# Kernel optimization log

Measured on AMD Instinct MI355X. Metric: run time of the kernel, lower is better.

Reference implementation:

```python
import jax, jax.numpy as jnp
import numpy as np

B, N, D = 4, 2048, 1024
HEADS, DIM_HEAD = 16, 64
INNER = HEADS * DIM_HEAD  # 1024
SCALE = DIM_HEAD ** -0.5


def setup_inputs() -> dict:
    key = jax.random.key(0)
    ks = jax.random.split(key, 8)
    w = 0.02
    return {
        "x":  jax.random.normal(ks[0], (B, N, D), dtype=jnp.float32),
        "Wq": jax.random.normal(ks[1], (D, INNER), dtype=jnp.float32) * w,
        "bq": jax.random.normal(ks[2], (INNER,), dtype=jnp.float32) * w,
        "Wv": jax.random.normal(ks[3], (D, INNER), dtype=jnp.float32) * w,
        "bv": jax.random.normal(ks[4], (INNER,), dtype=jnp.float32) * w,
        "Wo": jax.random.normal(ks[5], (INNER, D), dtype=jnp.float32) * w,
        "bo": jax.random.normal(ks[6], (D,), dtype=jnp.float32) * w,
    }


def reference(x, Wq, bq, Wv, bv, Wo, bo):
    b, n, _ = x.shape
    q = x @ Wq + bq                      # [b, n, inner]
    v = x @ Wv + bv                      # [b, n, inner]
    # split heads -> [b, h, n, d]
    q = q.reshape(b, n, HEADS, DIM_HEAD).transpose(0, 2, 1, 3).astype(jnp.float32)
    v = v.reshape(b, n, HEADS, DIM_HEAD).transpose(0, 2, 1, 3)
    # k = q (self L2 attention)
    AB = jnp.einsum('bhid,bhjd->bhij', q, q)          # [b, h, n, n]
    AA = jnp.sum(q * q, axis=-1, keepdims=True)       # [b, h, n, 1]
    BB = jnp.swapaxes(AA, -1, -2)                     # [b, h, 1, n]
    sim = -(AA - 2.0 * AB + BB) * SCALE               # negative scaled L2 distance
    attn = jax.nn.softmax(sim, axis=-1)
    out = jnp.einsum('bhij,bhjd->bhid', attn, v)      # [b, h, n, d]
    out = out.transpose(0, 2, 1, 3).reshape(b, n, INNER)
    return out @ Wo + bo
```

## Files before the change

kernel.cpp:

```cpp
#include <hip/hip_runtime.h>
#include <hip/hip_bf16.h>

#define SEQ 2048
#define SCALE 0.125f
#define LOG2E 1.4426950408889634f

typedef __bf16 bf16;
typedef __bf16 bf16x4 __attribute__((ext_vector_type(4)));
typedef __bf16 bf16x8 __attribute__((ext_vector_type(8)));
typedef float f32x4 __attribute__((ext_vector_type(4)));
typedef unsigned int u32;

__device__ __forceinline__ void gl_lds16(const void* g, void* l) {
    __builtin_amdgcn_global_load_lds((const __attribute__((address_space(1))) u32*)g,
                                     (__attribute__((address_space(3))) u32*)l, 16, 0, 0);
}


__global__ __launch_bounds__(256) void k_cast_x(const float4* __restrict__ x,
                                                bf16x4* __restrict__ xb) {
    int t = blockIdx.x * 256 + threadIdx.x;
    float4 f = x[t];
    bf16x4 o;
    o[0] = (bf16)f.x; o[1] = (bf16)f.y; o[2] = (bf16)f.z; o[3] = (bf16)f.w;
    xb[t] = o;
}

__global__ __launch_bounds__(256) void k_transpose_cast(const float* __restrict__ src,
                                                        bf16* __restrict__ dst) {
    __shared__ float tile[32][33];
    int bx = blockIdx.x * 32;
    int by = blockIdx.y * 32;
    int tx = threadIdx.x;
    int ty = threadIdx.y;
#pragma unroll
    for (int j = 0; j < 32; j += 8)
        tile[ty + j][tx] = src[(size_t)(by + ty + j) * 1024 + bx + tx];
    __syncthreads();
#pragma unroll
    for (int j = 0; j < 32; j += 8)
        dst[(size_t)(bx + ty + j) * 1024 + by + tx] = (bf16)tile[tx][ty + j];
}


__global__ __launch_bounds__(256) void k_gemm_qv(const bf16* __restrict__ Xb,
                                                 const bf16* __restrict__ Wqvt,
                                                 const float* __restrict__ bq,
                                                 const float* __restrict__ bv,
                                                 bf16* __restrict__ Q,
                                                 bf16* __restrict__ Vt,
                                                 float* __restrict__ QN) {
    constexpr int K = 1024;
    __shared__ bf16 As[128 * 32];
    __shared__ bf16 Bs[128 * 32];
    int t = threadIdx.x, w = t >> 6, l = t & 63;
    int blockN = blockIdx.x * 128, blockM = blockIdx.y * 128;
    int wm = w & 1, wn = w >> 1;
    int lr = l & 15, quad = l >> 4, q8 = quad * 8;
    int skcol = (l & 3) * 8;
    bool isQ = blockN < 1024;

    f32x4 acc[4][4] = {};
    const bf16* Ab = Xb + (size_t)blockM * K;
    const bf16* Bb = Wqvt + (size_t)blockN * K;

    for (int k0 = 0; k0 < K; k0 += 32) {
#pragma unroll
        for (int c2 = 0; c2 < 2; ++c2) {
            int c = 2 * w + c2;
            int row = c * 16 + (l >> 2);
            gl_lds16(Ab + (size_t)row * K + k0 + skcol, As + c * 512);
            gl_lds16(Bb + (size_t)row * K + k0 + skcol, Bs + c * 512);
        }
        __syncthreads();
        const bf16* Aw = As + wm * 64 * 32;
        const bf16* Bw = Bs + wn * 64 * 32;
        bf16x8 af[4], bfr[4];
#pragma unroll
        for (int mi = 0; mi < 4; ++mi) af[mi] = *(const bf16x8*)(Aw + (mi * 16 + lr) * 32 + q8);
#pragma unroll
        for (int ni = 0; ni < 4; ++ni) bfr[ni] = *(const bf16x8*)(Bw + (ni * 16 + lr) * 32 + q8);
        if (isQ) {
#pragma unroll
            for (int mi = 0; mi < 4; ++mi)
#pragma unroll
                for (int ni = 0; ni < 4; ++ni)
                    acc[mi][ni] = __builtin_amdgcn_mfma_f32_16x16x32_bf16(af[mi], bfr[ni], acc[mi][ni], 0, 0, 0);
        } else {
#pragma unroll
            for (int mi = 0; mi < 4; ++mi)
#pragma unroll
                for (int ni = 0; ni < 4; ++ni)
                    acc[mi][ni] = __builtin_amdgcn_mfma_f32_16x16x32_bf16(bfr[ni], af[mi], acc[mi][ni], 0, 0, 0);
        }
        __syncthreads();
    }

    int colbase = blockN + wn * 64;
    if (isQ) {
        int h = colbase >> 6;
        float bias[4];
#pragma unroll
        for (int ni = 0; ni < 4; ++ni) bias[ni] = bq[colbase + ni * 16 + lr];
#pragma unroll
        for (int mi = 0; mi < 4; ++mi) {
#pragma unroll
            for (int r = 0; r < 4; ++r) {
                int m = blockM + wm * 64 + mi * 16 + quad * 4 + r;
                int b = m >> 11, s = m & 2047;
                int bh = (b << 4) + h;
                float qsq = 0.f;
#pragma unroll
                for (int ni = 0; ni < 4; ++ni) {
                    float v = acc[mi][ni][r] + bias[ni];
                    bf16 vb = (bf16)v;
                    Q[((size_t)bh * SEQ + s) * 64 + ni * 16 + lr] = vb;
                    float vr = (float)vb;
                    qsq += vr * vr;
                }
                qsq += __shfl_xor(qsq, 1);
                qsq += __shfl_xor(qsq, 2);
                qsq += __shfl_xor(qsq, 4);
                qsq += __shfl_xor(qsq, 8);
                if (lr == 0) QN[(size_t)bh * SEQ + s] = qsq;
            }
        }
    } else {
        int h = (colbase - 1024) >> 6;
        int b = blockM >> 11;
        int bh = (b << 4) + h;
        int s_base = (blockM & 2047) + wm * 64;
        const float* bvh = bv + (colbase - 1024);
#pragma unroll
        for (int ni = 0; ni < 4; ++ni) {
#pragma unroll
            for (int r = 0; r < 4; ++r) {
                int dh = ni * 16 + quad * 4 + r;
                float bias = bvh[dh];
#pragma unroll
                for (int mi = 0; mi < 4; ++mi) {
                    int s = s_base + mi * 16 + lr;
                    Vt[((size_t)bh * 64 + dh) * SEQ + s] = (bf16)(acc[mi][ni][r] + bias);
                }
            }
        }
    }
}


__global__ __launch_bounds__(256, 3) void k_attn(const bf16* __restrict__ Q,
                                                 const bf16* __restrict__ Vt,
                                                 const float* __restrict__ QN,
                                                 bf16* __restrict__ AO) {
    __shared__ bf16 Ks[64 * 64];
    __shared__ bf16 Vs[64 * 64];
    __shared__ bf16 Ps[4][32 * 64];
    __shared__ float BBl[2048];

    int t = threadIdx.x, w = t >> 6, l = t & 63;
    int bh = blockIdx.y;
    int i0 = blockIdx.x * 128;
    const bf16* Qh = Q + (size_t)bh * SEQ * 64;
    const bf16* Vh = Vt + (size_t)bh * 64 * SEQ;
    int lr = l & 15, quad = l >> 4, q8 = quad * 8, lr7 = lr & 7;

    {
        const float4* QN4 = (const float4*)(QN + (size_t)bh * SEQ);
        float4* BB4 = (float4*)BBl;
#pragma unroll
        for (int i = 0; i < 2; ++i) {
            float4 v = QN4[t + i * 256];
            v.x *= (SCALE * LOG2E); v.y *= (SCALE * LOG2E);
            v.z *= (SCALE * LOG2E); v.w *= (SCALE * LOG2E);
            BB4[t + i * 256] = v;
        }
    }

    bf16x8 af[2][2];
#pragma unroll
    for (int mi = 0; mi < 2; ++mi)
#pragma unroll
        for (int kc = 0; kc < 2; ++kc)
            af[mi][kc] = *(const bf16x8*)(Qh + (size_t)(i0 + w * 32 + mi * 16 + lr) * 64 + kc * 32 + q8);

    f32x4 oacc[2][4] = {};
    float dpart[2][4] = {};

    int koff[2][4], poff[2][2];
#pragma unroll
    for (int kc = 0; kc < 2; ++kc) {
#pragma unroll
        for (int ni = 0; ni < 4; ++ni)
            koff[kc][ni] = (ni * 16 + lr) * 64 + (((kc * 4 + quad) ^ lr7) * 8);
#pragma unroll
        for (int mi = 0; mi < 2; ++mi)
            poff[kc][mi] = (mi * 16 + lr) * 64 + (((kc * 4 + quad) ^ lr7) * 8);
    }

    int s_r0 = t >> 3, s_c0 = t & 7;
    int s_r1 = s_r0 + 32;
    int s_l0 = s_r0 * 64 + ((s_c0 ^ (s_r0 & 7)) * 8);
    int s_l1 = s_r1 * 64 + ((s_c0 ^ (s_r1 & 7)) * 8);

    bf16* Pw = Ps[w];

    for (int j0 = 0; j0 < SEQ; j0 += 64) {
        __syncthreads();
        *(bf16x8*)(Ks + s_l0) = *(const bf16x8*)(Qh + (size_t)(j0 + s_r0) * 64 + s_c0 * 8);
        *(bf16x8*)(Ks + s_l1) = *(const bf16x8*)(Qh + (size_t)(j0 + s_r1) * 64 + s_c0 * 8);
        *(bf16x8*)(Vs + s_l0) = *(const bf16x8*)(Vh + (size_t)s_r0 * SEQ + j0 + s_c0 * 8);
        *(bf16x8*)(Vs + s_l1) = *(const bf16x8*)(Vh + (size_t)s_r1 * SEQ + j0 + s_c0 * 8);
        __syncthreads();

#pragma unroll
        for (int ni = 0; ni < 4; ++ni) {
            float bbt = BBl[j0 + ni * 16 + lr];
            bf16x8 bk0 = *(const bf16x8*)(Ks + koff[0][ni]);
            bf16x8 bk1 = *(const bf16x8*)(Ks + koff[1][ni]);
            f32x4 s0 = {}, s1 = {};
            s0 = __builtin_amdgcn_mfma_f32_16x16x32_bf16(af[0][0], bk0, s0, 0, 0, 0);
            s0 = __builtin_amdgcn_mfma_f32_16x16x32_bf16(af[0][1], bk1, s0, 0, 0, 0);
            s1 = __builtin_amdgcn_mfma_f32_16x16x32_bf16(af[1][0], bk0, s1, 0, 0, 0);
            s1 = __builtin_amdgcn_mfma_f32_16x16x32_bf16(af[1][1], bk1, s1, 0, 0, 0);
#pragma unroll
            for (int rr = 0; rr < 4; ++rr) {
                float p0 = __builtin_amdgcn_exp2f(s0[rr] * (2.f * SCALE * LOG2E) - bbt);
                float p1 = __builtin_amdgcn_exp2f(s1[rr] * (2.f * SCALE * LOG2E) - bbt);
                dpart[0][rr] += p0;
                dpart[1][rr] += p1;
                int row0 = quad * 4 + rr;
                int row1 = 16 + row0;
                Pw[row0 * 64 + (((ni * 2 + (lr >> 3)) ^ (row0 & 7)) * 8) + (lr & 7)] = (bf16)p0;
                Pw[row1 * 64 + (((ni * 2 + (lr >> 3)) ^ (row1 & 7)) * 8) + (lr & 7)] = (bf16)p1;
            }
        }

#pragma unroll
        for (int kc = 0; kc < 2; ++kc) {
            bf16x8 ap0 = *(const bf16x8*)(Pw + poff[kc][0]);
            bf16x8 ap1 = *(const bf16x8*)(Pw + poff[kc][1]);
#pragma unroll
            for (int di = 0; di < 4; ++di) {
                bf16x8 bv8 = *(const bf16x8*)(Vs + koff[kc][di]);
                oacc[0][di] = __builtin_amdgcn_mfma_f32_16x16x32_bf16(ap0, bv8, oacc[0][di], 0, 0, 0);
                oacc[1][di] = __builtin_amdgcn_mfma_f32_16x16x32_bf16(ap1, bv8, oacc[1][di], 0, 0, 0);
            }
        }
    }

    int b = bh >> 4, h = bh & 15;
#pragma unroll
    for (int mi = 0; mi < 2; ++mi) {
#pragma unroll
        for (int r = 0; r < 4; ++r) {
            float d = dpart[mi][r];
            d += __shfl_xor(d, 1);
            d += __shfl_xor(d, 2);
            d += __shfl_xor(d, 4);
            d += __shfl_xor(d, 8);
            float inv = 1.f / d;
            int s = i0 + w * 32 + mi * 16 + quad * 4 + r;
#pragma unroll
            for (int di = 0; di < 4; ++di) {
                AO[((size_t)(b * SEQ + s)) * 1024 + h * 64 + di * 16 + lr] = (bf16)(oacc[mi][di][r] * inv);
            }
        }
    }
}


__global__ __launch_bounds__(256) void k_gemm_out(const bf16* __restrict__ AO,
                                                  const bf16* __restrict__ Wot,
                                                  const float* __restrict__ bo,
                                                  float* __restrict__ out) {
    constexpr int K = 1024;
    __shared__ bf16 As[128 * 32];
    __shared__ bf16 Bs[128 * 32];
    int t = threadIdx.x, w = t >> 6, l = t & 63;
    int blockN = blockIdx.x * 128, blockM = blockIdx.y * 128;
    int wm = w & 1, wn = w >> 1;
    int lr = l & 15, quad = l >> 4, q8 = quad * 8;
    int skcol = (l & 3) * 8;

    f32x4 acc[4][4] = {};
    const bf16* Ab = AO + (size_t)blockM * K;
    const bf16* Bb = Wot + (size_t)blockN * K;

    for (int k0 = 0; k0 < K; k0 += 32) {
#pragma unroll
        for (int c2 = 0; c2 < 2; ++c2) {
            int c = 2 * w + c2;
            int row = c * 16 + (l >> 2);
            gl_lds16(Ab + (size_t)row * K + k0 + skcol, As + c * 512);
            gl_lds16(Bb + (size_t)row * K + k0 + skcol, Bs + c * 512);
        }
        __syncthreads();
        const bf16* Aw = As + wm * 64 * 32;
        const bf16* Bw = Bs + wn * 64 * 32;
        bf16x8 af[4], bfr[4];
#pragma unroll
        for (int mi = 0; mi < 4; ++mi) af[mi] = *(const bf16x8*)(Aw + (mi * 16 + lr) * 32 + q8);
#pragma unroll
        for (int ni = 0; ni < 4; ++ni) bfr[ni] = *(const bf16x8*)(Bw + (ni * 16 + lr) * 32 + q8);
#pragma unroll
        for (int mi = 0; mi < 4; ++mi)
#pragma unroll
            for (int ni = 0; ni < 4; ++ni)
                acc[mi][ni] = __builtin_amdgcn_mfma_f32_16x16x32_bf16(af[mi], bfr[ni], acc[mi][ni], 0, 0, 0);
        __syncthreads();
    }

    int colbase = blockN + wn * 64;
    float bias[4];
#pragma unroll
    for (int ni = 0; ni < 4; ++ni) bias[ni] = bo[colbase + ni * 16 + lr];
#pragma unroll
    for (int mi = 0; mi < 4; ++mi) {
#pragma unroll
        for (int r = 0; r < 4; ++r) {
            int m = blockM + wm * 64 + mi * 16 + quad * 4 + r;
#pragma unroll
            for (int ni = 0; ni < 4; ++ni) {
                out[(size_t)m * 1024 + colbase + ni * 16 + lr] = acc[mi][ni][r] + bias[ni];
            }
        }
    }
}


extern "C" void kernel_launch(void* const* d_in, const int* in_sizes, int n_in,
                              void* d_out, int out_size, void* d_ws, size_t ws_size,
                              hipStream_t stream) {
    const float* x  = (const float*)d_in[0];
    const float* Wq = (const float*)d_in[1];
    const float* bq = (const float*)d_in[2];
    const float* Wv = (const float*)d_in[3];
    const float* bv = (const float*)d_in[4];
    const float* Wo = (const float*)d_in[5];
    const float* bo = (const float*)d_in[6];
    float* out = (float*)d_out;

    char* ws = (char*)d_ws;
    bf16* Xb   = (bf16*)ws;
    bf16* Wqvt = (bf16*)(ws + (size_t)(16 << 20));
    bf16* Wot  = (bf16*)(ws + (size_t)(20 << 20));
    bf16* Qb   = (bf16*)(ws + (size_t)(22 << 20));
    bf16* Vtb  = (bf16*)(ws + (size_t)(38 << 20));
    float* QN  = (float*)(ws + (size_t)(54 << 20));
    bf16* AO   = Xb;

    k_cast_x<<<8192, 256, 0, stream>>>((const float4*)x, (bf16x4*)Xb);
    dim3 tb(32, 8);
    k_transpose_cast<<<dim3(32, 32), tb, 0, stream>>>(Wq, Wqvt);
    k_transpose_cast<<<dim3(32, 32), tb, 0, stream>>>(Wv, Wqvt + 1024 * 1024);
    k_transpose_cast<<<dim3(32, 32), tb, 0, stream>>>(Wo, Wot);
    k_gemm_qv<<<dim3(16, 64), 256, 0, stream>>>(Xb, Wqvt, bq, bv, Qb, Vtb, QN);
    k_attn<<<dim3(16, 64), 256, 0, stream>>>(Qb, Vtb, QN, AO);
    k_gemm_out<<<dim3(8, 64), 256, 0, stream>>>(AO, Wot, bo, out);
}
```

Before: 307.1 us.

## Keep attention probabilities in registers via transposed QK MFMA and fp16 PV

The attention kernel now computes the score tile transposed (K as the A operand), so each lane's exp outputs line up directly with the A-operand layout of a 16x16x16 fp16 MFMA. This removes the per-warp LDS round trip for P. V is stored in fp16 with a padded LDS layout. Next-tile K/V global loads are prefetched into registers while the current tile is computed, occupancy is raised to 4 blocks per CU, and the row sums are reduced through a small LDS buffer. The cost is lower fp16 precision for P and V and twice as many smaller MFMAs for the PV product.

```diff
diff --git a/kernel.cpp b/kernel.cpp
--- a/kernel.cpp
+++ b/kernel.cpp
@@ -8,8 +8,16 @@
 typedef __bf16 bf16;
 typedef __bf16 bf16x4 __attribute__((ext_vector_type(4)));
 typedef __bf16 bf16x8 __attribute__((ext_vector_type(8)));
+typedef _Float16 f16;
+typedef _Float16 f16x2 __attribute__((ext_vector_type(2)));
+typedef _Float16 f16x4 __attribute__((ext_vector_type(4)));
 typedef float f32x4 __attribute__((ext_vector_type(4)));
 typedef unsigned int u32;
+typedef unsigned int u32x4 __attribute__((ext_vector_type(4)));
+
+__device__ __forceinline__ f16x2 pk_f16(float a, float b) {
+    return __builtin_bit_cast(f16x2, __builtin_amdgcn_cvt_pkrtz(a, b));
+}
 
 __device__ __forceinline__ void gl_lds16(const void* g, void* l) {
     __builtin_amdgcn_global_load_lds((const __attribute__((address_space(1))) u32*)g,
@@ -48,7 +56,7 @@
                                                  const float* __restrict__ bq,
                                                  const float* __restrict__ bv,
                                                  bf16* __restrict__ Q,
-                                                 bf16* __restrict__ Vt,
+                                                 f16* __restrict__ Vt,
                                                  float* __restrict__ QN) {
     constexpr int K = 1024;
     __shared__ bf16 As[128 * 32];
@@ -140,7 +148,7 @@
 #pragma unroll
                 for (int mi = 0; mi < 4; ++mi) {
                     int s = s_base + mi * 16 + lr;
-                    Vt[((size_t)bh * 64 + dh) * SEQ + s] = (bf16)(acc[mi][ni][r] + bias);
+                    Vt[((size_t)bh * 64 + dh) * SEQ + s] = (f16)(acc[mi][ni][r] + bias);
                 }
             }
         }
@@ -148,20 +156,20 @@
 }
 
 
-__global__ __launch_bounds__(256, 3) void k_attn(const bf16* __restrict__ Q,
-                                                 const bf16* __restrict__ Vt,
+__global__ __launch_bounds__(256, 4) void k_attn(const bf16* __restrict__ Q,
+                                                 const f16* __restrict__ Vt,
                                                  const float* __restrict__ QN,
                                                  bf16* __restrict__ AO) {
     __shared__ bf16 Ks[64 * 64];
-    __shared__ bf16 Vs[64 * 64];
-    __shared__ bf16 Ps[4][32 * 64];
+    __shared__ f16 Vs[64 * 72];
     __shared__ float BBl[2048];
+    __shared__ float Dl[4][32];
 
     int t = threadIdx.x, w = t >> 6, l = t & 63;
     int bh = blockIdx.y;
     int i0 = blockIdx.x * 128;
     const bf16* Qh = Q + (size_t)bh * SEQ * 64;
-    const bf16* Vh = Vt + (size_t)bh * 64 * SEQ;
+    const f16* Vh = Vt + (size_t)bh * 64 * SEQ;
     int lr = l & 15, quad = l >> 4, q8 = quad * 8, lr7 = lr & 7;
 
     {
@@ -184,81 +192,98 @@
             af[mi][kc] = *(const bf16x8*)(Qh + (size_t)(i0 + w * 32 + mi * 16 + lr) * 64 + kc * 32 + q8);
 
     f32x4 oacc[2][4] = {};
-    float dpart[2][4] = {};
-
-    int koff[2][4], poff[2][2];
-#pragma unroll
-    for (int kc = 0; kc < 2; ++kc) {
-#pragma unroll
-        for (int ni = 0; ni < 4; ++ni)
-            koff[kc][ni] = (ni * 16 + lr) * 64 + (((kc * 4 + quad) ^ lr7) * 8);
-#pragma unroll
-        for (int mi = 0; mi < 2; ++mi)
-            poff[kc][mi] = (mi * 16 + lr) * 64 + (((kc * 4 + quad) ^ lr7) * 8);
-    }
-
-    int s_r0 = t >> 3, s_c0 = t & 7;
-    int s_r1 = s_r0 + 32;
-    int s_l0 = s_r0 * 64 + ((s_c0 ^ (s_r0 & 7)) * 8);
-    int s_l1 = s_r1 * 64 + ((s_c0 ^ (s_r1 & 7)) * 8);
-
-    bf16* Pw = Ps[w];
+    float dpart[2] = {0.f, 0.f};
+
+    int kb[2];
+#pragma unroll
+    for (int kc = 0; kc < 2; ++kc) kb[kc] = lr * 64 + (((kc * 4 + quad) ^ lr7) * 8);
+    int vb[4];
+#pragma unroll
+    for (int di = 0; di < 4; ++di) vb[di] = (di * 16 + lr) * 72 + quad * 4;
+
+    int sr0 = t >> 3, sc0 = t & 7;
+    int sr1 = sr0 + 32;
+    int ksl0 = sr0 * 64 + ((sc0 ^ (sr0 & 7)) * 8);
+    int ksl1 = sr1 * 64 + ((sc0 ^ (sr1 & 7)) * 8);
+    int vsl0 = sr0 * 72 + sc0 * 8;
+    int vsl1 = sr1 * 72 + sc0 * 8;
+
+    u32x4 rk0 = *(const u32x4*)(Qh + (size_t)sr0 * 64 + sc0 * 8);
+    u32x4 rk1 = *(const u32x4*)(Qh + (size_t)sr1 * 64 + sc0 * 8);
+    u32x4 rv0 = *(const u32x4*)(Vh + (size_t)sr0 * SEQ + sc0 * 8);
+    u32x4 rv1 = *(const u32x4*)(Vh + (size_t)sr1 * SEQ + sc0 * 8);
+
+    const float c2s = 2.f * SCALE * LOG2E;
 
     for (int j0 = 0; j0 < SEQ; j0 += 64) {
         __syncthreads();
-        *(bf16x8*)(Ks + s_l0) = *(const bf16x8*)(Qh + (size_t)(j0 + s_r0) * 64 + s_c0 * 8);
-        *(bf16x8*)(Ks + s_l1) = *(const bf16x8*)(Qh + (size_t)(j0 + s_r1) * 64 + s_c0 * 8);
-        *(bf16x8*)(Vs + s_l0) = *(const bf16x8*)(Vh + (size_t)s_r0 * SEQ + j0 + s_c0 * 8);
-        *(bf16x8*)(Vs + s_l1) = *(const bf16x8*)(Vh + (size_t)s_r1 * SEQ + j0 + s_c0 * 8);
+        *(u32x4*)(Ks + ksl0) = rk0;
+        *(u32x4*)(Ks + ksl1) = rk1;
+        *(u32x4*)(Vs + vsl0) = rv0;
+        *(u32x4*)(Vs + vsl1) = rv1;
+        int jn = j0 + 64;
+        if (jn < SEQ) {
+            rk0 = *(const u32x4*)(Qh + (size_t)(jn + sr0) * 64 + sc0 * 8);
+            rk1 = *(const u32x4*)(Qh + (size_t)(jn + sr1) * 64 + sc0 * 8);
+            rv0 = *(const u32x4*)(Vh + (size_t)sr0 * SEQ + jn + sc0 * 8);
+            rv1 = *(const u32x4*)(Vh + (size_t)sr1 * SEQ + jn + sc0 * 8);
+        }
         __syncthreads();
 
 #pragma unroll
         for (int ni = 0; ni < 4; ++ni) {
-            float bbt = BBl[j0 + ni * 16 + lr];
-            bf16x8 bk0 = *(const bf16x8*)(Ks + koff[0][ni]);
-            bf16x8 bk1 = *(const bf16x8*)(Ks + koff[1][ni]);
-            f32x4 s0 = {}, s1 = {};
-            s0 = __builtin_amdgcn_mfma_f32_16x16x32_bf16(af[0][0], bk0, s0, 0, 0, 0);
-            s0 = __builtin_amdgcn_mfma_f32_16x16x32_bf16(af[0][1], bk1, s0, 0, 0, 0);
-            s1 = __builtin_amdgcn_mfma_f32_16x16x32_bf16(af[1][0], bk0, s1, 0, 0, 0);
-            s1 = __builtin_amdgcn_mfma_f32_16x16x32_bf16(af[1][1], bk1, s1, 0, 0, 0);
-#pragma unroll
-            for (int rr = 0; rr < 4; ++rr) {
-                float p0 = __builtin_amdgcn_exp2f(s0[rr] * (2.f * SCALE * LOG2E) - bbt);
-                float p1 = __builtin_amdgcn_exp2f(s1[rr] * (2.f * SCALE * LOG2E) - bbt);
-                dpart[0][rr] += p0;
-                dpart[1][rr] += p1;
-                int row0 = quad * 4 + rr;
-                int row1 = 16 + row0;
-                Pw[row0 * 64 + (((ni * 2 + (lr >> 3)) ^ (row0 & 7)) * 8) + (lr & 7)] = (bf16)p0;
-                Pw[row1 * 64 + (((ni * 2 + (lr >> 3)) ^ (row1 & 7)) * 8) + (lr & 7)] = (bf16)p1;
-            }
-        }
-
-#pragma unroll
-        for (int kc = 0; kc < 2; ++kc) {
-            bf16x8 ap0 = *(const bf16x8*)(Pw + poff[kc][0]);
-            bf16x8 ap1 = *(const bf16x8*)(Pw + poff[kc][1]);
+            bf16x8 bk0 = *(const bf16x8*)(Ks + ni * 1024 + kb[0]);
+            bf16x8 bk1 = *(const bf16x8*)(Ks + ni * 1024 + kb[1]);
+            f32x4 sT0 = {}, sT1 = {};
+            sT0 = __builtin_amdgcn_mfma_f32_16x16x32_bf16(bk0, af[0][0], sT0, 0, 0, 0);
+            sT0 = __builtin_amdgcn_mfma_f32_16x16x32_bf16(bk1, af[0][1], sT0, 0, 0, 0);
+            sT1 = __builtin_amdgcn_mfma_f32_16x16x32_bf16(bk0, af[1][0], sT1, 0, 0, 0);
+            sT1 = __builtin_amdgcn_mfma_f32_16x16x32_bf16(bk1, af[1][1], sT1, 0, 0, 0);
+
+            f32x4 bbt = *(const f32x4*)(BBl + j0 + ni * 16 + quad * 4);
+
+            float p00 = __builtin_amdgcn_exp2f(sT0[0] * c2s - bbt[0]);
+            float p01 = __builtin_amdgcn_exp2f(sT0[1] * c2s - bbt[1]);
+            float p02 = __builtin_amdgcn_exp2f(sT0[2] * c2s - bbt[2]);
+            float p03 = __builtin_amdgcn_exp2f(sT0[3] * c2s - bbt[3]);
+            float p10 = __builtin_amdgcn_exp2f(sT1[0] * c2s - bbt[0]);
+            float p11 = __builtin_amdgcn_exp2f(sT1[1] * c2s - bbt[1]);
+            float p12 = __builtin_amdgcn_exp2f(sT1[2] * c2s - bbt[2]);
+            float p13 = __builtin_amdgcn_exp2f(sT1[3] * c2s - bbt[3]);
+            dpart[0] += (p00 + p01) + (p02 + p03);
+            dpart[1] += (p10 + p11) + (p12 + p13);
+
+            f16x2 a0 = pk_f16(p00, p01);
+            f16x2 a1 = pk_f16(p02, p03);
+            f16x2 b0 = pk_f16(p10, p11);
+            f16x2 b1 = pk_f16(p12, p13);
+            f16x4 pf0 = {a0[0], a0[1], a1[0], a1[1]};
+            f16x4 pf1 = {b0[0], b0[1], b1[0], b1[1]};
+
 #pragma unroll
             for (int di = 0; di < 4; ++di) {
-                bf16x8 bv8 = *(const bf16x8*)(Vs + koff[kc][di]);
-                oacc[0][di] = __builtin_amdgcn_mfma_f32_16x16x32_bf16(ap0, bv8, oacc[0][di], 0, 0, 0);
-                oacc[1][di] = __builtin_amdgcn_mfma_f32_16x16x32_bf16(ap1, bv8, oacc[1][di], 0, 0, 0);
-            }
-        }
-    }
+                f16x4 vf = *(const f16x4*)(Vs + vb[di] + ni * 16);
+                oacc[0][di] = __builtin_amdgcn_mfma_f32_16x16x16f16(pf0, vf, oacc[0][di], 0, 0, 0);
+                oacc[1][di] = __builtin_amdgcn_mfma_f32_16x16x16f16(pf1, vf, oacc[1][di], 0, 0, 0);
+            }
+        }
+    }
+
+#pragma unroll
+    for (int mi = 0; mi < 2; ++mi) {
+        float ds = dpart[mi];
+        ds += __shfl_xor(ds, 16);
+        ds += __shfl_xor(ds, 32);
+        if (quad == 0) Dl[w][mi * 16 + lr] = ds;
+    }
+    __syncthreads();
 
     int b = bh >> 4, h = bh & 15;
 #pragma unroll
     for (int mi = 0; mi < 2; ++mi) {
 #pragma unroll
         for (int r = 0; r < 4; ++r) {
-            float d = dpart[mi][r];
-            d += __shfl_xor(d, 1);
-            d += __shfl_xor(d, 2);
-            d += __shfl_xor(d, 4);
-            d += __shfl_xor(d, 8);
-            float inv = 1.f / d;
+            float inv = 1.f / Dl[w][mi * 16 + quad * 4 + r];
             int s = i0 + w * 32 + mi * 16 + quad * 4 + r;
 #pragma unroll
             for (int di = 0; di < 4; ++di) {
@@ -345,7 +370,7 @@
     bf16* Wqvt = (bf16*)(ws + (size_t)(16 << 20));
     bf16* Wot  = (bf16*)(ws + (size_t)(20 << 20));
     bf16* Qb   = (bf16*)(ws + (size_t)(22 << 20));
-    bf16* Vtb  = (bf16*)(ws + (size_t)(38 << 20));
+    f16*  Vtb  = (f16*)(ws + (size_t)(38 << 20));
     float* QN  = (float*)(ws + (size_t)(54 << 20));
     bf16* AO   = Xb;
 
```

New measurement: 307.0 us. About the same (-0.0%).
